# Kernel optimization log

Hardware: AMD Instinct MI355X
Metric: run time of the kernel (lower is better)

## Reference

```python
import jax, jax.numpy as jnp
import numpy as np

N, D, H, F = 50000, 128, 8, 512
HD = D // H
EPS_BN = 1e-5


def _batchnorm(x, gamma, beta):
    # BatchNorm1d in training mode: per-feature batch stats over node dim
    m = x.mean(axis=0)
    v = x.var(axis=0)
    return (x - m) * jax.lax.rsqrt(v + EPS_BN) * gamma + beta


def setup_inputs() -> dict:
    key = jax.random.key(0)
    ks = jax.random.split(key, 12)
    s = 0.05
    return {
        "src": jax.random.normal(ks[0], (N, D), jnp.float32),
        "edge_index": jax.random.randint(ks[1], (2, 800000), 0, N, jnp.int64),
        "q_w": jax.random.normal(ks[2], (D, D), jnp.float32) * s,
        "q_b": jnp.zeros((D,), jnp.float32),
        "k_w": jax.random.normal(ks[3], (D, D), jnp.float32) * s,
        "v_w": jax.random.normal(ks[4], (D, D), jnp.float32) * s,
        "out_w": jax.random.normal(ks[5], (D, D), jnp.float32) * s,
        "out_b": jnp.zeros((D,), jnp.float32),
        "g1": jnp.ones((D,), jnp.float32),
        "b1": jnp.zeros((D,), jnp.float32),
        "lin1_w": jax.random.normal(ks[6], (F, D), jnp.float32) * s,
        "lin1_b": jnp.zeros((F,), jnp.float32),
        "lin2_w": jax.random.normal(ks[7], (D, F), jnp.float32) * s,
        "lin2_b": jnp.zeros((D,), jnp.float32),
        "g2": jnp.ones((D,), jnp.float32),
        "b2": jnp.zeros((D,), jnp.float32),
    }


def reference(src, edge_index, q_w, q_b, k_w, v_w, out_w, out_b,
              g1, b1, lin1_w, lin1_b, lin2_w, lin2_b, g2, b2):
    n = src.shape[0]
    # add self loops, then attention edge index is (dst=edge[1], src=edge[0])
    loops = jnp.arange(n, dtype=edge_index.dtype)
    ei = jnp.concatenate([edge_index, jnp.stack([loops, loops])], axis=1)
    e_src, e_dst = ei[0], ei[1]  # message flows e_src -> e_dst; query index = e_dst

    scaling = float(HD) ** (-0.5)
    q = ((src @ q_w.T + q_b) * scaling).reshape(n, H, HD)
    k = (src @ k_w.T).reshape(n, H, HD)
    v = (src @ v_w.T).reshape(n, H, HD)

    # per-edge scores [E, H]
    w = jnp.einsum("ehd,ehd->eh", q[e_dst], k[e_src])
    # deterministic segment softmax over edges grouped by destination node
    mx = jax.ops.segment_max(w, e_dst, num_segments=n)
    ex = jnp.exp(w - mx[e_dst])
    den = jax.ops.segment_sum(ex, e_dst, num_segments=n)
    attn_w = ex / (den[e_dst] + 1e-16)  # [E, H]

    # weighted scatter-add aggregation -> [n, H, HD]
    msgs = attn_w[:, :, None] * v[e_src]
    agg = jax.ops.segment_sum(msgs, e_dst, num_segments=n)

    attn_out = agg.reshape(n, D) @ out_w.T + out_b
    x = _batchnorm(src + attn_out, g1, b1)

    ff = jax.nn.leaky_relu(x @ lin1_w.T + lin1_b, negative_slope=0.01)
    ff = ff @ lin2_w.T + lin2_b
    x = _batchnorm(x + ff, g2, b2)
    return x
```

## Files before the change

### kernel.cpp

```cpp
#include <hip/hip_runtime.h>
#include <math.h>

#define D 128
#define H 8
#define HD 16

typedef __attribute__((ext_vector_type(8))) short bf16x8;
typedef __attribute__((ext_vector_type(4))) float f32x4;

__device__ __forceinline__ ushort f2bf(float x) {
    union { float f; unsigned u; } v; v.f = x;
    unsigned r = v.u + 0x7fffu + ((v.u >> 16) & 1u);
    return (ushort)(r >> 16);
}
__device__ __forceinline__ float bflo(unsigned u) {
    union { unsigned u; float f; } x; x.u = u << 16; return x.f;
}
__device__ __forceinline__ float bfhi(unsigned u) {
    union { unsigned u; float f; } x; x.u = u & 0xffff0000u; return x.f;
}
__device__ __forceinline__ float bf2f(short s) {
    union { unsigned u; float f; } x; x.u = ((unsigned)(ushort)s) << 16; return x.f;
}

__device__ __forceinline__ float dot16(const float* qf, uint4 a, uint4 b) {
    float w;
    w  = qf[0]  * bflo(a.x) + qf[1]  * bfhi(a.x);
    w += qf[2]  * bflo(a.y) + qf[3]  * bfhi(a.y);
    w += qf[4]  * bflo(a.z) + qf[5]  * bfhi(a.z);
    w += qf[6]  * bflo(a.w) + qf[7]  * bfhi(a.w);
    w += qf[8]  * bflo(b.x) + qf[9]  * bfhi(b.x);
    w += qf[10] * bflo(b.y) + qf[11] * bfhi(b.y);
    w += qf[12] * bflo(b.z) + qf[13] * bfhi(b.z);
    w += qf[14] * bflo(b.w) + qf[15] * bfhi(b.w);
    return w;
}
__device__ __forceinline__ void acc16(float* num, float e, uint4 a, uint4 b) {
    num[0]  = fmaf(e, bflo(a.x), num[0]);  num[1]  = fmaf(e, bfhi(a.x), num[1]);
    num[2]  = fmaf(e, bflo(a.y), num[2]);  num[3]  = fmaf(e, bfhi(a.y), num[3]);
    num[4]  = fmaf(e, bflo(a.z), num[4]);  num[5]  = fmaf(e, bfhi(a.z), num[5]);
    num[6]  = fmaf(e, bflo(a.w), num[6]);  num[7]  = fmaf(e, bfhi(a.w), num[7]);
    num[8]  = fmaf(e, bflo(b.x), num[8]);  num[9]  = fmaf(e, bfhi(b.x), num[9]);
    num[10] = fmaf(e, bflo(b.y), num[10]); num[11] = fmaf(e, bfhi(b.y), num[11]);
    num[12] = fmaf(e, bflo(b.z), num[12]); num[13] = fmaf(e, bfhi(b.z), num[13]);
    num[14] = fmaf(e, bflo(b.w), num[14]); num[15] = fmaf(e, bfhi(b.w), num[15]);
}

template<int EPI, int M, int STATS>
__global__ __launch_bounds__(256)
void gemm_v4_kernel(const ushort* __restrict__ A,
                    const ushort* __restrict__ W,
                    const float* __restrict__ bias,
                    const float* __restrict__ extf,
                    ushort* __restrict__ outb,
                    float* __restrict__ stats,
                    int N)
{
    const int lane = threadIdx.x & 63, wave = threadIdx.x >> 6;
    const int lr = lane & 15, lq = lane >> 4;
    const int colbase = blockIdx.y * 128 + wave * 32;

    bf16x8 bfr[2][4];
    {
        const ushort* wp = W + (size_t)(colbase + lr) * 128 + lq * 8;
        #pragma unroll
        for (int ct = 0; ct < 2; ++ct)
            #pragma unroll
            for (int t = 0; t < 4; ++t)
                bfr[ct][t] = *(const bf16x8*)(wp + (size_t)ct * 16 * 128 + t * 32);
    }
    float biasv[2];
    biasv[0] = bias[colbase + lr];
    biasv[1] = bias[colbase + 16 + lr];

    float ssum[2] = {0.f, 0.f}, ssq[2] = {0.f, 0.f};

    const int stride = gridDim.x * 32;
    int r0 = blockIdx.x * 32;
    if (r0 < N) {
        bf16x8 cur[2][4], nxt[2][4];
        auto loadA = [&](int rb, bf16x8 (&dst)[2][4]) {
            #pragma unroll
            for (int s = 0; s < 2; ++s) {
                int ar = min(rb + s * 16 + lr, N - 1);
                const ushort* ap = A + (size_t)ar * 128 + lq * 8;
                #pragma unroll
                for (int t = 0; t < 4; ++t)
                    dst[s][t] = *(const bf16x8*)(ap + t * 32);
            }
        };
        loadA(r0, cur);

        while (true) {
            int rn = r0 + stride;
            if (rn < N) loadA(rn, nxt);

            f32x4 acc[2][2] = {};
            #pragma unroll
            for (int t = 0; t < 4; ++t) {
                acc[0][0] = __builtin_amdgcn_mfma_f32_16x16x32_bf16(cur[0][t], bfr[0][t], acc[0][0], 0, 0, 0);
                acc[1][0] = __builtin_amdgcn_mfma_f32_16x16x32_bf16(cur[1][t], bfr[0][t], acc[1][0], 0, 0, 0);
                acc[0][1] = __builtin_amdgcn_mfma_f32_16x16x32_bf16(cur[0][t], bfr[1][t], acc[0][1], 0, 0, 0);
                acc[1][1] = __builtin_amdgcn_mfma_f32_16x16x32_bf16(cur[1][t], bfr[1][t], acc[1][1], 0, 0, 0);
            }

            #pragma unroll
            for (int ct = 0; ct < 2; ++ct) {
                int gcol = colbase + ct * 16 + lr;
                #pragma unroll
                for (int s = 0; s < 2; ++s) {
                    #pragma unroll
                    for (int r = 0; r < 4; ++r) {
                        int grow = r0 + s * 16 + lq * 4 + r;
                        if (grow >= N) continue;
                        size_t o = (size_t)grow * M + gcol;
                        float v = acc[s][ct][r] + biasv[ct];
                        if (EPI == 2)      v = v > 0.f ? v : 0.01f * v;
                        else if (EPI == 3) v += extf[o];
                        if (STATS) { ssum[ct] += v; ssq[ct] = fmaf(v, v, ssq[ct]); }
                        outb[o] = f2bf(v);
                    }
                }
            }

            if (rn >= N) break;
            r0 = rn;
            #pragma unroll
            for (int s = 0; s < 2; ++s)
                #pragma unroll
                for (int t = 0; t < 4; ++t) cur[s][t] = nxt[s][t];
        }
    }

    if (STATS) {
        #pragma unroll
        for (int ct = 0; ct < 2; ++ct) {
            float a = ssum[ct], b = ssq[ct];
            a += __shfl_xor(a, 16, 64);  b += __shfl_xor(b, 16, 64);
            a += __shfl_xor(a, 32, 64);  b += __shfl_xor(b, 32, 64);
            if (lq == 0) {
                unsafeAtomicAdd(&stats[colbase + ct * 16 + lr], a);
                unsafeAtomicAdd(&stats[128 + colbase + ct * 16 + lr], b);
            }
        }
    }
}

template<int K, int MW>
__global__ __launch_bounds__(256)
void gemm_v2_kernel(const ushort* __restrict__ Ap,
                    const ushort* __restrict__ W,
                    const float* __restrict__ bias,
                    const ushort* __restrict__ extb,
                    const float* __restrict__ rawstats,
                    const float* __restrict__ gg,
                    const float* __restrict__ bb,
                    ushort* __restrict__ outb,
                    int N)
{
    constexpr int M   = MW * 4;
    constexpr int KC  = 128;
    constexpr int KT  = KC / 32;
    constexpr int NKC = K / KC;

    const int lane = threadIdx.x & 63, wave = threadIdx.x >> 6;
    const int lr = lane & 15, lq = lane >> 4;
    const int row0 = blockIdx.x * 16;
    const int c0w  = wave * MW;

    int ar0 = min(row0 + lr, N - 1);

    bf16x8 afr[KT];
    auto loadA = [&](int kc) {
        const ushort* ap = Ap + (size_t)ar0 * K + kc * KC + lq * 8;
        #pragma unroll
        for (int t = 0; t < KT; ++t) afr[t] = *(const bf16x8*)(ap + t * 32);
    };

    f32x4 acc[2] = {};
    #pragma unroll 1
    for (int kc = 0; kc < NKC; ++kc) {
        loadA(kc);
        const ushort* wp0 = W + (size_t)(c0w + lr) * K + kc * KC + lq * 8;
        const ushort* wp1 = wp0 + (size_t)16 * K;
        #pragma unroll
        for (int t = 0; t < KT; ++t) {
            bf16x8 b0 = *(const bf16x8*)(wp0 + t * 32);
            bf16x8 b1 = *(const bf16x8*)(wp1 + t * 32);
            acc[0] = __builtin_amdgcn_mfma_f32_16x16x32_bf16(afr[t], b0, acc[0], 0, 0, 0);
            acc[1] = __builtin_amdgcn_mfma_f32_16x16x32_bf16(afr[t], b1, acc[1], 0, 0, 0);
        }
    }

    #pragma unroll
    for (int ct = 0; ct < 2; ++ct) {
        int col = c0w + ct * 16 + lr;
        float biasv = bias[col];
        float mean = rawstats[col] / (float)N;
        float var  = rawstats[128 + col] / (float)N - mean * mean;
        float scv = gg[col] * rsqrtf(var + 1e-5f);
        float shv = bb[col] - mean * scv;
        #pragma unroll
        for (int r = 0; r < 4; ++r) {
            int grow = row0 + lq * 4 + r;
            if (grow >= N) continue;
            size_t o = (size_t)grow * M + col;
            float v = acc[ct][r] + biasv + fmaf(bf2f((short)extb[o]), scv, shv);
            outb[o] = f2bf(v);
        }
    }
}

__global__ __launch_bounds__(256)
void convert_deg_kernel(const float* __restrict__ qw, const float* __restrict__ qb,
                        const float* __restrict__ kw, const float* __restrict__ vw,
                        const float* __restrict__ ow, const float* __restrict__ w1,
                        const float* __restrict__ w2,
                        ushort* __restrict__ wqkv, ushort* __restrict__ wout,
                        ushort* __restrict__ w1b, ushort* __restrict__ w2b,
                        float* __restrict__ bqkv,
                        const float* __restrict__ src, ushort* __restrict__ srcbf,
                        int nd8,
                        const int* __restrict__ ei, long long E0,
                        int* __restrict__ deg)
{
    long long i = (long long)blockIdx.x * 256 + threadIdx.x;
    if (i < E0) atomicAdd(&deg[ei[E0 + i]], 1);
    if (i < nd8) {
        const float4* sp = (const float4*)(src + i * 8);
        float4 f0 = sp[0], f1 = sp[1];
        ushort u[8];
        u[0]=f2bf(f0.x); u[1]=f2bf(f0.y); u[2]=f2bf(f0.z); u[3]=f2bf(f0.w);
        u[4]=f2bf(f1.x); u[5]=f2bf(f1.y); u[6]=f2bf(f1.z); u[7]=f2bf(f1.w);
        *(uint4*)(srcbf + i * 8) = *(uint4*)u;
    }
    if (i < 49152) {
        int row = (int)i >> 7;
        float v;
        if (row < 128)      v = 0.25f * qw[i];
        else if (row < 256) v = kw[i - 16384];
        else                v = vw[i - 32768];
        wqkv[i] = f2bf(v);
        return;
    }
    long long j = i - 49152;
    if (j < 16384) { wout[j] = f2bf(ow[j]); return; }
    j -= 16384;
    if (j < 65536) { w1b[j] = f2bf(w1[j]); return; }
    j -= 65536;
    if (j < 65536) { w2b[j] = f2bf(w2[j]); return; }
    j -= 65536;
    if (j < 384) bqkv[j] = (j < 128) ? 0.25f * qb[j] : 0.f;
}

__global__ __launch_bounds__(256)
void w1fold_kernel(const ushort* __restrict__ w1b, const float* __restrict__ lb1,
                   const float* __restrict__ rawstats,
                   const float* __restrict__ g1, const float* __restrict__ b1,
                   ushort* __restrict__ w1f, float* __restrict__ bias1f, int N)
{
    int f = blockIdx.x * 4 + (threadIdx.x >> 6);
    int lane = threadIdx.x & 63;
    int k0 = lane * 2;
    float m0 = rawstats[k0] / (float)N;
    float v0 = rawstats[128 + k0] / (float)N - m0 * m0;
    float sc0 = g1[k0] * rsqrtf(v0 + 1e-5f);
    float sh0 = b1[k0] - m0 * sc0;
    float m1 = rawstats[k0 + 1] / (float)N;
    float v1 = rawstats[128 + k0 + 1] / (float)N - m1 * m1;
    float sc1 = g1[k0 + 1] * rsqrtf(v1 + 1e-5f);
    float sh1 = b1[k0 + 1] - m1 * sc1;

    uint wp = *(const uint*)(w1b + (size_t)f * 128 + k0);
    float w0 = bflo(wp), w1v = bfhi(wp);
    uint o = (uint)f2bf(w0 * sc0) | ((uint)f2bf(w1v * sc1) << 16);
    *(uint*)(w1f + (size_t)f * 128 + k0) = o;

    float part = w0 * sh0 + w1v * sh1;
    #pragma unroll
    for (int m = 1; m < 64; m <<= 1) part += __shfl_xor(part, m, 64);
    if (lane == 0) bias1f[f] = lb1[f] + part;
}

__global__ __launch_bounds__(256)
void scan_block_sum(const int* __restrict__ deg, int n, int* __restrict__ bsum)
{
    __shared__ int sh[256];
    int i = blockIdx.x * 256 + threadIdx.x;
    sh[threadIdx.x] = (i < n) ? deg[i] : 0;
    __syncthreads();
    for (int ofs = 128; ofs > 0; ofs >>= 1) {
        if (threadIdx.x < ofs) sh[threadIdx.x] += sh[threadIdx.x + ofs];
        __syncthreads();
    }
    if (threadIdx.x == 0) bsum[blockIdx.x] = sh[0];
}

__global__ __launch_bounds__(256)
void scan_final(const int* __restrict__ deg, int n, const int* __restrict__ bsum,
                int nb, int* __restrict__ rowptr)
{
    __shared__ int sb[256];
    __shared__ int sh[256];
    int t = threadIdx.x;
    sb[t] = (t < nb) ? bsum[t] : 0;
    __syncthreads();
    for (int ofs = 1; ofs < 256; ofs <<= 1) {
        int v = (t >= ofs) ? sb[t - ofs] : 0;
        __syncthreads();
        sb[t] += v;
        __syncthreads();
    }
    int boff = (blockIdx.x == 0) ? 0 : sb[blockIdx.x - 1];

    int i = blockIdx.x * 256 + t;
    int v = (i < n) ? deg[i] : 0;
    sh[t] = v;
    __syncthreads();
    for (int ofs = 1; ofs < 256; ofs <<= 1) {
        int u = (t >= ofs) ? sh[t - ofs] : 0;
        __syncthreads();
        sh[t] += u;
        __syncthreads();
    }
    if (i < n) rowptr[i] = boff + sh[t] - v;
    if (i == n - 1) rowptr[n] = boff + sh[t];
}

__global__ __launch_bounds__(256)
void scatter_kernel(const int* __restrict__ ei, long long E0,
                    const int* __restrict__ rowptr, int* __restrict__ cnt,
                    int* __restrict__ col)
{
    long long e = (long long)blockIdx.x * 256 + threadIdx.x;
    if (e >= E0) return;
    int s = ei[e], d = ei[E0 + e];
    int pos = rowptr[d] + atomicAdd(&cnt[d], 1);
    col[pos] = s;
}

__global__ __launch_bounds__(256)
void gat_agg_kernel(const int* __restrict__ rowptr, const int* __restrict__ col,
                    const ushort* __restrict__ qkv, ushort* __restrict__ agg, int N)
{
    int node = blockIdx.x * 4 + (threadIdx.x >> 6);
    if (node >= N) return;
    int lane = threadIdx.x & 63;
    int es = lane >> 3, h = lane & 7;
    const uint4* Q = (const uint4*)qkv;

    const uint4* qp = Q + (size_t)node * 48 + h * 2;
    uint4 qa = qp[0], qb = qp[1];
    float qf[16];
    qf[0]=bflo(qa.x); qf[1]=bfhi(qa.x); qf[2]=bflo(qa.y); qf[3]=bfhi(qa.y);
    qf[4]=bflo(qa.z); qf[5]=bfhi(qa.z); qf[6]=bflo(qa.w); qf[7]=bfhi(qa.w);
    qf[8]=bflo(qb.x); qf[9]=bfhi(qb.x); qf[10]=bflo(qb.y); qf[11]=bfhi(qb.y);
    qf[12]=bflo(qb.z); qf[13]=bfhi(qb.z); qf[14]=bflo(qb.w); qf[15]=bfhi(qb.w);

    float num[16];
    #pragma unroll
    for (int i = 0; i < 16; i++) num[i] = 0.f;
    float den = 0.f;

    int beg = rowptr[node];
    int total = rowptr[node + 1] - beg + 1;
    for (int idx = es; idx < total; idx += 8) {
        int s = (idx == 0) ? node : col[beg + idx - 1];
        const uint4* rp = Q + (size_t)s * 48 + h * 2;
        uint4 ka = rp[16], kb = rp[17], va = rp[32], vb = rp[33];
        float ev = __expf(dot16(qf, ka, kb));
        den += ev;
        acc16(num, ev, va, vb);
    }

    #pragma unroll
    for (int m = 8; m < 64; m <<= 1) {
        den += __shfl_xor(den, m, 64);
        #pragma unroll
        for (int i = 0; i < 16; i++) num[i] += __shfl_xor(num[i], m, 64);
    }

    if (es == 0) {
        float inv = 1.f / (den + 1e-16f);
        uint4 o0, o1;
        o0.x = (uint)f2bf(num[0]*inv)  | ((uint)f2bf(num[1]*inv)  << 16);
        o0.y = (uint)f2bf(num[2]*inv)  | ((uint)f2bf(num[3]*inv)  << 16);
        o0.z = (uint)f2bf(num[4]*inv)  | ((uint)f2bf(num[5]*inv)  << 16);
        o0.w = (uint)f2bf(num[6]*inv)  | ((uint)f2bf(num[7]*inv)  << 16);
        o1.x = (uint)f2bf(num[8]*inv)  | ((uint)f2bf(num[9]*inv)  << 16);
        o1.y = (uint)f2bf(num[10]*inv) | ((uint)f2bf(num[11]*inv) << 16);
        o1.z = (uint)f2bf(num[12]*inv) | ((uint)f2bf(num[13]*inv) << 16);
        o1.w = (uint)f2bf(num[14]*inv) | ((uint)f2bf(num[15]*inv) << 16);
        uint4* op = (uint4*)(agg + (size_t)node * 128 + h * 16);
        op[0] = o0; op[1] = o1;
    }
}

__global__ __launch_bounds__(256)
void bn_stats_bf16_kernel(const ushort* __restrict__ y, int N, float* __restrict__ stats)
{
    int jp = threadIdx.x & 63;
    int q4 = threadIdx.x >> 6;
    int r = blockIdx.x * 256 + q4;
    int rend = min(N, (int)(blockIdx.x + 1) * 256);
    float s0 = 0.f, qq0 = 0.f, s1 = 0.f, qq1 = 0.f;
    const uint* yp = (const uint*)y;
    for (; r < rend; r += 4) {
        uint u = yp[(size_t)r * 64 + jp];
        float a = bflo(u), b = bfhi(u);
        s0 += a; qq0 += a * a; s1 += b; qq1 += b * b;
    }
    __shared__ float sh[4][64][4];
    sh[q4][jp][0] = s0; sh[q4][jp][1] = qq0; sh[q4][jp][2] = s1; sh[q4][jp][3] = qq1;
    __syncthreads();
    if (threadIdx.x < 128) {
        int p = threadIdx.x >> 1;
        int w = threadIdx.x & 1;
        float ss = 0.f, sq = 0.f;
        #pragma unroll
        for (int i = 0; i < 4; i++) { ss += sh[i][p][w * 2]; sq += sh[i][p][w * 2 + 1]; }
        unsafeAtomicAdd(&stats[2 * p + w], ss);
        unsafeAtomicAdd(&stats[128 + 2 * p + w], sq);
    }
}

__global__ __launch_bounds__(256)
void bn_apply_out_kernel(const ushort* __restrict__ y, const float* __restrict__ rawstats,
                         const float* __restrict__ g, const float* __restrict__ b,
                         float* __restrict__ out, int total4, int N)
{
    __shared__ float scs[128], shs[128];
    if (threadIdx.x < 128) {
        int j = threadIdx.x;
        float mean = rawstats[j] / (float)N;
        float var  = rawstats[128 + j] / (float)N - mean * mean;
        float sc = g[j] * rsqrtf(var + 1e-5f);
        scs[j] = sc;
        shs[j] = b[j] - mean * sc;
    }
    __syncthreads();
    int i = blockIdx.x * 256 + threadIdx.x;
    if (i >= total4) return;
    uint2 u = reinterpret_cast<const uint2*>(y)[i];
    int j = (i * 4) & (D - 1);
    float4 v;
    v.x = bflo(u.x) * scs[j + 0] + shs[j + 0];
    v.y = bfhi(u.x) * scs[j + 1] + shs[j + 1];
    v.z = bflo(u.y) * scs[j + 2] + shs[j + 2];
    v.w = bfhi(u.y) * scs[j + 3] + shs[j + 3];
    reinterpret_cast<float4*>(out)[i] = v;
}

extern "C" void kernel_launch(void* const* d_in, const int* in_sizes, int n_in,
                              void* d_out, int out_size, void* d_ws, size_t ws_size,
                              hipStream_t stream)
{
    const float* src    = (const float*)d_in[0];
    const int*   ei     = (const int*)  d_in[1];
    const float* q_w    = (const float*)d_in[2];
    const float* q_b    = (const float*)d_in[3];
    const float* k_w    = (const float*)d_in[4];
    const float* v_w    = (const float*)d_in[5];
    const float* out_w  = (const float*)d_in[6];
    const float* out_b  = (const float*)d_in[7];
    const float* g1     = (const float*)d_in[8];
    const float* b1     = (const float*)d_in[9];
    const float* lin1_w = (const float*)d_in[10];
    const float* lin1_b = (const float*)d_in[11];
    const float* lin2_w = (const float*)d_in[12];
    const float* lin2_b = (const float*)d_in[13];
    const float* g2     = (const float*)d_in[14];
    const float* b2     = (const float*)d_in[15];

    const int N        = in_sizes[0] / D;
    const long long E0 = in_sizes[1] / 2;

    float* ws = (float*)d_ws;
    size_t off = 0;
    ushort* qkv   = (ushort*)(ws + off); off += (size_t)N * 192;
    ushort* agg   = (ushort*)(ws + off); off += (size_t)N * 64;
    ushort* srcbf = (ushort*)(ws + off); off += (size_t)N * 64;
    ushort* y1b   = (ushort*)(ws + off); off += (size_t)N * 64;
    ushort* hid   = (ushort*)(ws + off); off += (size_t)N * 256;
    ushort* y2b   = (ushort*)(ws + off); off += (size_t)N * 64;
    ushort* wqkv  = (ushort*)(ws + off); off += 24576;
    ushort* woutb = (ushort*)(ws + off); off += 8192;
    ushort* w1b   = (ushort*)(ws + off); off += 32768;
    ushort* w1f   = (ushort*)(ws + off); off += 32768;
    ushort* w2b   = (ushort*)(ws + off); off += 32768;
    float*  bqkv  = ws + off;            off += 384;
    float*  bias1f= ws + off;            off += 512;
    size_t zero_start = off;
    int* deg    = (int*)(ws + off); off += N;
    int* cnt    = (int*)(ws + off); off += N;
    float* stats1 = ws + off; off += 512;
    float* stats2 = ws + off; off += 512;
    size_t zero_cnt = off - zero_start;
    int* rowptr = (int*)(ws + off); off += N + 1;
    int* bsum   = (int*)(ws + off); off += 256;
    int* col    = (int*)(ws + off); off += E0;

    hipMemsetAsync(ws + zero_start, 0, zero_cnt * sizeof(float), stream);

    dim3 blk(256);

    dim3 gE0((unsigned)((E0 + 255) / 256));
    hipLaunchKernelGGL(convert_deg_kernel, gE0, blk, 0, stream,
                       q_w, q_b, k_w, v_w, out_w, lin1_w, lin2_w,
                       wqkv, woutb, w1b, w2b, bqkv,
                       src, srcbf, N * 16, ei, E0, deg);

    int nb = (N + 255) / 256;
    hipLaunchKernelGGL(scan_block_sum, dim3(nb), blk, 0, stream, deg, N, bsum);
    hipLaunchKernelGGL(scan_final, dim3(nb), blk, 0, stream, deg, N, bsum, nb, rowptr);
    hipLaunchKernelGGL(scatter_kernel, gE0, blk, 0, stream, ei, E0, rowptr, cnt, col);

    const int gx = 1024;

    hipLaunchKernelGGL((gemm_v4_kernel<0, 384, 0>), dim3(gx, 3), blk, 0, stream,
                       srcbf, wqkv, bqkv, nullptr, qkv, nullptr, N);

    hipLaunchKernelGGL(gat_agg_kernel, dim3((N + 3) / 4), blk, 0, stream,
                       rowptr, col, qkv, agg, N);

    hipLaunchKernelGGL((gemm_v4_kernel<3, 128, 1>), dim3(gx, 1), blk, 0, stream,
                       agg, woutb, out_b, src, y1b, stats1, N);

    hipLaunchKernelGGL(w1fold_kernel, dim3(128), blk, 0, stream,
                       w1b, lin1_b, stats1, g1, b1, w1f, bias1f, N);

    hipLaunchKernelGGL((gemm_v4_kernel<2, 512, 0>), dim3(gx, 4), blk, 0, stream,
                       y1b, w1f, bias1f, nullptr, hid, nullptr, N);

    hipLaunchKernelGGL((gemm_v2_kernel<512, 32>), dim3((N + 15) / 16), blk, 0, stream,
                       hid, w2b, lin2_b, y1b, stats1, g1, b1, y2b, N);

    dim3 gS((N + 255) / 256);
    hipLaunchKernelGGL(bn_stats_bf16_kernel, gS, blk, 0, stream, y2b, N, stats2);
    int total4 = N * D / 4;
    hipLaunchKernelGGL(bn_apply_out_kernel, dim3((total4 + 255) / 256), blk, 0, stream,
                       y2b, stats2, g2, b2, (float*)d_out, total4, N);
}
```

Baseline: 463.5 us.

## Stage lin2 A tile in LDS via async global_load_lds with 32-row blocks

Replaces the templated lin2 GEMM with a specialized kernel that processes 32 rows per block instead of 16. The block's whole A tile (32x512 bf16) is loaded into LDS with asynchronous global-to-LDS loads and an XOR swizzle to avoid bank conflicts. W fragments are double-buffered in registers so the next K-chunk loads while the current MFMAs run. Each W fragment now feeds two row sub-tiles, halving W traffic per row, at the cost of 32KB of LDS per block and possibly lower occupancy.

```diff
diff --git a/kernel.cpp b/kernel.cpp
--- a/kernel.cpp
+++ b/kernel.cpp
@@ -7,6 +7,9 @@
 
 typedef __attribute__((ext_vector_type(8))) short bf16x8;
 typedef __attribute__((ext_vector_type(4))) float f32x4;
+
+#define GLOBAL_AS __attribute__((address_space(1)))
+#define LDS_AS    __attribute__((address_space(3)))
 
 __device__ __forceinline__ ushort f2bf(float x) {
     union { float f; unsigned u; } v; v.f = x;
@@ -146,9 +149,8 @@
     }
 }
 
-template<int K, int MW>
-__global__ __launch_bounds__(256)
-void gemm_v2_kernel(const ushort* __restrict__ Ap,
+__global__ __launch_bounds__(256)
+void lin2_v6_kernel(const ushort* __restrict__ Ap,
                     const ushort* __restrict__ W,
                     const float* __restrict__ bias,
                     const ushort* __restrict__ extb,
@@ -158,39 +160,66 @@
                     ushort* __restrict__ outb,
                     int N)
 {
-    constexpr int M   = MW * 4;
-    constexpr int KC  = 128;
-    constexpr int KT  = KC / 32;
-    constexpr int NKC = K / KC;
+    constexpr int K = 512;
+    __shared__ ushort alds[32 * K];
 
     const int lane = threadIdx.x & 63, wave = threadIdx.x >> 6;
     const int lr = lane & 15, lq = lane >> 4;
-    const int row0 = blockIdx.x * 16;
-    const int c0w  = wave * MW;
-
-    int ar0 = min(row0 + lr, N - 1);
-
-    bf16x8 afr[KT];
-    auto loadA = [&](int kc) {
-        const ushort* ap = Ap + (size_t)ar0 * K + kc * KC + lq * 8;
-        #pragma unroll
-        for (int t = 0; t < KT; ++t) afr[t] = *(const bf16x8*)(ap + t * 32);
+    const int row0 = blockIdx.x * 32;
+    const int c0w  = wave * 32;
+
+    #pragma unroll
+    for (int i = 0; i < 8; ++i) {
+        int r = wave * 8 + i;
+        int gr = min(row0 + r, N - 1);
+        const ushort* gsrc = Ap + (size_t)gr * K + (size_t)((lane ^ (r & 7)) * 8);
+        __builtin_amdgcn_global_load_lds(
+            (const GLOBAL_AS void*)gsrc,
+            (LDS_AS void*)(alds + (size_t)r * K),
+            16, 0, 0);
+    }
+
+    bf16x8 wA[8], wB[8];
+    auto loadW = [&](int kc, bf16x8 (&wd)[8]) {
+        const ushort* wp0 = W + (size_t)(c0w + lr) * K + kc * 128 + lq * 8;
+        #pragma unroll
+        for (int t = 0; t < 4; ++t) {
+            wd[t]     = *(const bf16x8*)(wp0 + t * 32);
+            wd[4 + t] = *(const bf16x8*)(wp0 + (size_t)16 * K + t * 32);
+        }
     };
-
-    f32x4 acc[2] = {};
-    #pragma unroll 1
-    for (int kc = 0; kc < NKC; ++kc) {
-        loadA(kc);
-        const ushort* wp0 = W + (size_t)(c0w + lr) * K + kc * KC + lq * 8;
-        const ushort* wp1 = wp0 + (size_t)16 * K;
-        #pragma unroll
-        for (int t = 0; t < KT; ++t) {
-            bf16x8 b0 = *(const bf16x8*)(wp0 + t * 32);
-            bf16x8 b1 = *(const bf16x8*)(wp1 + t * 32);
-            acc[0] = __builtin_amdgcn_mfma_f32_16x16x32_bf16(afr[t], b0, acc[0], 0, 0, 0);
-            acc[1] = __builtin_amdgcn_mfma_f32_16x16x32_bf16(afr[t], b1, acc[1], 0, 0, 0);
+    loadW(0, wA);
+    loadW(1, wB);
+
+    __syncthreads();
+
+    f32x4 acc[2][2] = {};
+    bf16x8 a[2][4];
+    auto ldsA = [&](int kc) {
+        #pragma unroll
+        for (int s = 0; s < 2; ++s) {
+            const ushort* lp = alds + (size_t)(s * 16 + lr) * K;
+            #pragma unroll
+            for (int t = 0; t < 4; ++t)
+                a[s][t] = *(const bf16x8*)(lp + (kc * 16 + ((t * 4 + lq) ^ (lr & 7))) * 8);
         }
-    }
+    };
+    auto mf = [&](bf16x8 (&wd)[8]) {
+        #pragma unroll
+        for (int t = 0; t < 4; ++t) {
+            acc[0][0] = __builtin_amdgcn_mfma_f32_16x16x32_bf16(a[0][t], wd[t],     acc[0][0], 0, 0, 0);
+            acc[1][0] = __builtin_amdgcn_mfma_f32_16x16x32_bf16(a[1][t], wd[t],     acc[1][0], 0, 0, 0);
+            acc[0][1] = __builtin_amdgcn_mfma_f32_16x16x32_bf16(a[0][t], wd[4 + t], acc[0][1], 0, 0, 0);
+            acc[1][1] = __builtin_amdgcn_mfma_f32_16x16x32_bf16(a[1][t], wd[4 + t], acc[1][1], 0, 0, 0);
+        }
+    };
+
+    ldsA(0); mf(wA);
+    loadW(2, wA);
+    ldsA(1); mf(wB);
+    loadW(3, wB);
+    ldsA(2); mf(wA);
+    ldsA(3); mf(wB);
 
     #pragma unroll
     for (int ct = 0; ct < 2; ++ct) {
@@ -201,12 +230,15 @@
         float scv = gg[col] * rsqrtf(var + 1e-5f);
         float shv = bb[col] - mean * scv;
         #pragma unroll
-        for (int r = 0; r < 4; ++r) {
-            int grow = row0 + lq * 4 + r;
-            if (grow >= N) continue;
-            size_t o = (size_t)grow * M + col;
-            float v = acc[ct][r] + biasv + fmaf(bf2f((short)extb[o]), scv, shv);
-            outb[o] = f2bf(v);
+        for (int s = 0; s < 2; ++s) {
+            #pragma unroll
+            for (int r = 0; r < 4; ++r) {
+                int grow = row0 + s * 16 + lq * 4 + r;
+                if (grow >= N) continue;
+                size_t o = (size_t)grow * 128 + col;
+                float v = acc[s][ct][r] + biasv + fmaf(bf2f((short)extb[o]), scv, shv);
+                outb[o] = f2bf(v);
+            }
         }
     }
 }
@@ -532,7 +564,7 @@
     hipLaunchKernelGGL((gemm_v4_kernel<2, 512, 0>), dim3(gx, 4), blk, 0, stream,
                        y1b, w1f, bias1f, nullptr, hid, nullptr, N);
 
-    hipLaunchKernelGGL((gemm_v2_kernel<512, 32>), dim3((N + 15) / 16), blk, 0, stream,
+    hipLaunchKernelGGL(lin2_v6_kernel, dim3((N + 31) / 32), blk, 0, stream,
                        hid, w2b, lin2_b, y1b, stats1, g1, b1, y2b, N);
 
     dim3 gS((N + 255) / 256);
```

Measured after the change: 427.5 us. 1.08x faster.
